# Optimization experiments

Hardware: AMD Instinct MI355X
Metric: run time of the kernel (lower is better)

Reference implementation:

```python
import jax, jax.numpy as jnp
import numpy as np

VOCAB, D_MODEL, N_HEADS, D_FF = 32000, 2048, 16, 8192
B, S = 2, 2048
HEAD_DIM = D_MODEL // N_HEADS
EPS = 1e-6


def setup_inputs() -> dict:
    key = jax.random.key(0)
    ks = jax.random.split(key, 12)
    sc = 0.02
    return {
        "tokens": jax.random.randint(ks[0], (B, S), 0, VOCAB),
        "tok_emb": jax.random.normal(ks[1], (VOCAB, D_MODEL), jnp.float32) * sc,
        "wq": jax.random.normal(ks[2], (D_MODEL, D_MODEL), jnp.float32) * sc,
        "wk": jax.random.normal(ks[3], (D_MODEL, D_MODEL), jnp.float32) * sc,
        "wv": jax.random.normal(ks[4], (D_MODEL, D_MODEL), jnp.float32) * sc,
        "wo": jax.random.normal(ks[5], (D_MODEL, D_MODEL), jnp.float32) * sc,
        "attn_norm_w": jnp.ones((D_MODEL,), jnp.float32),
        "ffn_norm_w": jnp.ones((D_MODEL,), jnp.float32),
        "final_norm_w": jnp.ones((D_MODEL,), jnp.float32),
        "w1": jax.random.normal(ks[6], (D_FF, D_MODEL), jnp.float32) * sc,
        "w2": jax.random.normal(ks[7], (D_MODEL, D_FF), jnp.float32) * sc,
        "out_proj": jax.random.normal(ks[8], (VOCAB, D_MODEL), jnp.float32) * sc,
    }


def rms_norm(x, w):
    return w * x * jax.lax.rsqrt(jnp.mean(x * x, axis=-1, keepdims=True) + EPS)


def reference(tokens, tok_emb, wq, wk, wv, wo, attn_norm_w, ffn_norm_w,
              final_norm_w, w1, w2, out_proj):
    x = tok_emb[tokens]  # [B, S, D]
    b, s, _ = x.shape

    # --- attention (explicit causal QK^T + softmax, as in source) ---
    xn = rms_norm(x, attn_norm_w)
    q = (xn @ wq.T).reshape(b, s, N_HEADS, HEAD_DIM)
    k = (xn @ wk.T).reshape(b, s, N_HEADS, HEAD_DIM)
    v = (xn @ wv.T).reshape(b, s, N_HEADS, HEAD_DIM)
    scores = jnp.einsum("bqhd,bkhd->bhqk", q, k) * (HEAD_DIM ** -0.5)
    causal = jnp.triu(jnp.ones((s, s), dtype=bool), k=1)  # True above diag
    scores = jnp.where(causal, -jnp.inf, scores)
    attn = jax.nn.softmax(scores, axis=-1)
    out = jnp.einsum("bhqk,bkhd->bqhd", attn, v).reshape(b, s, -1)
    x = x + out @ wo.T

    # --- FFN (world_size=1: all_gather/reduce_scatter are identities) ---
    hn = rms_norm(x, ffn_norm_w)
    h = jax.nn.silu(hn @ w1.T) @ w2.T
    x = x + h

    logits = rms_norm(x, final_norm_w) @ out_proj.T  # [B, S, VOCAB]
    return logits
```

## Files before the change

### kernel.cpp

```cpp
#include <hip/hip_runtime.h>
#include <stdint.h>

#define DM     2048
#define NHE    16
#define DFF    8192
#define NBATCH 2
#define SEQ    2048
#define NTOK   4096
#define HD     128
#define NVOCAB 32000

typedef __attribute__((ext_vector_type(8))) short short8;
typedef __attribute__((ext_vector_type(4))) float f32x4;
typedef __attribute__((ext_vector_type(4))) unsigned short u16x4;

static __device__ __forceinline__ unsigned short f2b(float f) {
  union { float f; uint32_t u; } v; v.f = f;
  return (unsigned short)((v.u + 0x7FFFu + ((v.u >> 16) & 1u)) >> 16);
}

static __device__ __forceinline__ void gload16(const void* g, void* l) {
  __builtin_amdgcn_global_load_lds(
      (const __attribute__((address_space(1))) unsigned int*)g,
      (__attribute__((address_space(3))) unsigned int*)l, 16, 0, 0);
}

__global__ void k_f32_to_bf16(const float* __restrict__ in,
                              unsigned short* __restrict__ out, int nq) {
  int i = blockIdx.x * blockDim.x + threadIdx.x;
  int stride = gridDim.x * blockDim.x;
  for (; i < nq; i += stride) {
    float4 v = ((const float4*)in)[i];
    u16x4 o;
    o.x = f2b(v.x); o.y = f2b(v.y); o.z = f2b(v.z); o.w = f2b(v.w);
    ((u16x4*)out)[i] = o;
  }
}

__global__ void k_embed(const int* __restrict__ tok,
                        const float* __restrict__ emb, float* __restrict__ x) {
  int n = blockIdx.x;
  int t = tok[n];
  const float4* src = (const float4*)(emb + (size_t)t * DM);
  float4* dst = (float4*)(x + (size_t)n * DM);
  for (int i = threadIdx.x; i < DM / 4; i += blockDim.x) dst[i] = src[i];
}

__global__ void k_rmsnorm(const float* __restrict__ x, const float* __restrict__ wt,
                          unsigned short* __restrict__ out) {
  int n = blockIdx.x;
  const float* row = x + (size_t)n * DM;
  float ss = 0.f;
  #pragma unroll
  for (int it = 0; it < 2; ++it) {
    int i = threadIdx.x * 4 + it * 1024;
    float4 v = *(const float4*)(row + i);
    ss += v.x * v.x + v.y * v.y + v.z * v.z + v.w * v.w;
  }
  #pragma unroll
  for (int m = 1; m < 64; m <<= 1) ss += __shfl_xor(ss, m);
  __shared__ float p[4];
  if ((threadIdx.x & 63) == 0) p[threadIdx.x >> 6] = ss;
  __syncthreads();
  float inv = rsqrtf((p[0] + p[1] + p[2] + p[3]) * (1.f / DM) + 1e-6f);
  #pragma unroll
  for (int it = 0; it < 2; ++it) {
    int i = threadIdx.x * 4 + it * 1024;
    float4 v = *(const float4*)(row + i);
    float4 w4 = *(const float4*)(wt + i);
    u16x4 o;
    o.x = f2b(v.x * w4.x * inv); o.y = f2b(v.y * w4.y * inv);
    o.z = f2b(v.z * w4.z * inv); o.w = f2b(v.w * w4.w * inv);
    *(u16x4*)(out + (size_t)n * DM + i) = o;
  }
}

#define EPI_BF16  0
#define EPI_RESID 1
#define EPI_SILU  2
#define EPI_F32   3

template <int EPI>
__launch_bounds__(512, 2)
__global__ void k_gemm_nt(const unsigned short* __restrict__ A,
                          const unsigned short* __restrict__ Bm,
                          int M, int N, int K,
                          float* __restrict__ Cf, unsigned short* __restrict__ Cb,
                          const float* __restrict__ R) {
  __shared__ unsigned short lds[2][32768];
  int nbn = N >> 8;
  int nwg = gridDim.x;
  int bid = blockIdx.x;
  int cpx = nwg >> 3;
  bid = (bid & 7) * cpx + (bid >> 3);
  int bm = bid / nbn, bn = bid % nbn;
  int t = threadIdx.x, w = t >> 6, lane = t & 63;
  int wr = w >> 2, wc = w & 3;
  int g = lane >> 4, l15 = lane & 15;

  f32x4 acc[8][4] = {};

  size_t abase = (size_t)(bm * 256) * K;
  size_t bbase = (size_t)(bn * 256) * K;
  int nkt = K >> 6;

  auto stage = [&](int buf, int kt) {
    unsigned short* dst = lds[buf];
    int k0 = kt << 6;
    #pragma unroll
    for (int i = 0; i < 4; ++i) {
      int pos = (i * 512 + t) << 4;
      int row = pos >> 7, colb = pos & 127;
      int csrc = colb ^ ((row & 7) << 4);
      gload16(A + abase + (size_t)row * K + k0 + (csrc >> 1), (char*)dst + pos);
    }
    #pragma unroll
    for (int i = 0; i < 4; ++i) {
      int pos = (i * 512 + t) << 4;
      int row = pos >> 7, colb = pos & 127;
      int csrc = colb ^ ((row & 7) << 4);
      gload16(Bm + bbase + (size_t)row * K + k0 + (csrc >> 1),
              (char*)(dst + 16384) + pos);
    }
  };

  stage(0, 0);
  for (int kt = 0; kt < nkt; ++kt) {
    int cur = kt & 1;
    if (kt + 1 < nkt) {
      stage(1 - cur, kt + 1);
      asm volatile("s_waitcnt vmcnt(8)" ::: "memory");
    } else {
      asm volatile("s_waitcnt vmcnt(0)" ::: "memory");
    }
    __builtin_amdgcn_s_barrier();
    __builtin_amdgcn_sched_barrier(0);

    const unsigned short* abuf = lds[cur];
    const unsigned short* bbuf = abuf + 16384;
    __builtin_amdgcn_s_setprio(1);
    #pragma unroll
    for (int kk = 0; kk < 2; ++kk) {
      short8 af[8], bfr[4];
      #pragma unroll
      for (int mm = 0; mm < 8; ++mm) {
        int row = wr * 128 + mm * 16 + l15;
        int col = kk * 64 + g * 16;
        af[mm] = *(const short8*)((const char*)abuf + row * 128 + (col ^ ((row & 7) << 4)));
      }
      #pragma unroll
      for (int nn = 0; nn < 4; ++nn) {
        int row = wc * 64 + nn * 16 + l15;
        int col = kk * 64 + g * 16;
        bfr[nn] = *(const short8*)((const char*)bbuf + row * 128 + (col ^ ((row & 7) << 4)));
      }
      #pragma unroll
      for (int mm = 0; mm < 8; ++mm)
        #pragma unroll
        for (int nn = 0; nn < 4; ++nn)
          acc[mm][nn] = __builtin_amdgcn_mfma_f32_16x16x32_bf16(af[mm], bfr[nn], acc[mm][nn], 0, 0, 0);
    }
    __builtin_amdgcn_s_setprio(0);
    __builtin_amdgcn_sched_barrier(0);
    __builtin_amdgcn_s_barrier();
  }

  #pragma unroll
  for (int mm = 0; mm < 8; ++mm) {
    #pragma unroll
    for (int nn = 0; nn < 4; ++nn) {
      #pragma unroll
      for (int r = 0; r < 4; ++r) {
        int grow = bm * 256 + wr * 128 + mm * 16 + g * 4 + r;
        int gcol = bn * 256 + wc * 64 + nn * 16 + l15;
        size_t off = (size_t)grow * N + gcol;
        float v = acc[mm][nn][r];
        if (EPI == EPI_BF16) {
          Cb[off] = f2b(v);
        } else if (EPI == EPI_RESID) {
          Cf[off] = R[off] + v;
        } else if (EPI == EPI_SILU) {
          float s = 1.f / (1.f + __expf(-v));
          Cb[off] = f2b(v * s);
        } else {
          Cf[off] = v;
        }
      }
    }
  }
}

__global__ void k_transpose_v(const unsigned short* __restrict__ v, int vstride,
                              unsigned short* __restrict__ vt) {
  __shared__ unsigned short tile[64][136];
  int pr = blockIdx.x >> 5;
  int st = blockIdx.x & 31;
  int bb = pr >> 4, h = pr & 15;
  int row = threadIdx.x >> 2;
  int cq = threadIdx.x & 3;
  const unsigned short* src =
      v + (size_t)(bb * SEQ + st * 64 + row) * vstride + h * HD + cq * 32;
  #pragma unroll
  for (int j = 0; j < 4; ++j)
    *(short8*)&tile[row][cq * 32 + j * 8] = *(const short8*)(src + j * 8);
  __syncthreads();
  int d = threadIdx.x >> 1;
  int sh = threadIdx.x & 1;
  unsigned short tmp[32];
  #pragma unroll
  for (int j = 0; j < 32; ++j) tmp[j] = tile[sh * 32 + j][d];
  unsigned short* dst = vt + ((size_t)pr * HD + d) * SEQ + st * 64 + sh * 32;
  #pragma unroll
  for (int j = 0; j < 4; ++j)
    *(short8*)(dst + j * 8) = *(const short8*)&tmp[j * 8];
}

__launch_bounds__(256)
__global__ void k_attn(const unsigned short* __restrict__ q,
                       const unsigned short* __restrict__ k,
                       const unsigned short* __restrict__ vt,
                       unsigned short* __restrict__ ao, int qk_stride) {
  __shared__ unsigned short k_lds[64 * 128];
  __shared__ unsigned short vt_lds[128 * 64];
  __shared__ unsigned short p_lds[4][32 * 64];

  int bid = blockIdx.x;
  int pr = bid >> 4;
  int qt = 15 - (bid & 15);
  int bb = pr >> 4, h = pr & 15;
  int t = threadIdx.x, w = t >> 6, lane = t & 63;
  int g = lane >> 4, l15 = lane & 15;
  const float SCL = 0.08838834764831845f * 1.4426950408889634f;

  int qrow_base = qt * 128 + w * 32;
  short8 aq[2][4];
  #pragma unroll
  for (int mm = 0; mm < 2; ++mm) {
    size_t n = (size_t)(bb * SEQ + qrow_base + mm * 16 + l15);
    #pragma unroll
    for (int kk = 0; kk < 4; ++kk)
      aq[mm][kk] = *(const short8*)(q + n * qk_stride + h * HD + kk * 32 + g * 8);
  }

  f32x4 o[2][8] = {};
  float m2[2][4], ls[2][4];
  #pragma unroll
  for (int mm = 0; mm < 2; ++mm)
    #pragma unroll
    for (int r = 0; r < 4; ++r) { m2[mm][r] = -1e30f; ls[mm][r] = 0.f; }

  int nkv = 2 * qt + 2;
  for (int kvt = 0; kvt < nkv; ++kvt) {
    #pragma unroll
    for (int i = 0; i < 4; ++i) {
      int pos = ((i * 4 + w) << 10) + lane * 16;
      {
        int row = pos >> 8, csw = pos & 255;
        int csrc = csw ^ ((row & 7) << 4);
        gload16(k + (size_t)(bb * SEQ + kvt * 64 + row) * qk_stride + h * HD + (csrc >> 1),
                (char*)k_lds + ((i * 4 + w) << 10));
      }
      {
        int row = pos >> 7, csw = pos & 127;
        int csrc = csw ^ ((row & 7) << 4);
        gload16(vt + ((size_t)pr * HD + row) * SEQ + kvt * 64 + (csrc >> 1),
                (char*)vt_lds + ((i * 4 + w) << 10));
      }
    }
    __syncthreads();

    f32x4 s[2][4] = {};
    #pragma unroll
    for (int kk = 0; kk < 4; ++kk) {
      short8 bk[4];
      #pragma unroll
      for (int nn = 0; nn < 4; ++nn) {
        int row = nn * 16 + l15;
        int col = kk * 64 + g * 16;
        bk[nn] = *(const short8*)((const char*)k_lds + row * 256 + (col ^ ((row & 7) << 4)));
      }
      #pragma unroll
      for (int mm = 0; mm < 2; ++mm)
        #pragma unroll
        for (int nn = 0; nn < 4; ++nn)
          s[mm][nn] = __builtin_amdgcn_mfma_f32_16x16x32_bf16(aq[mm][kk], bk[nn], s[mm][nn], 0, 0, 0);
    }

    bool diag = (kvt >= 2 * qt);
    #pragma unroll
    for (int mm = 0; mm < 2; ++mm) {
      float mx[4] = {-1e30f, -1e30f, -1e30f, -1e30f};
      #pragma unroll
      for (int nn = 0; nn < 4; ++nn)
        #pragma unroll
        for (int r = 0; r < 4; ++r) {
          float sv = s[mm][nn][r] * SCL;
          if (diag) {
            int kvg = kvt * 64 + nn * 16 + l15;
            int qg = qrow_base + mm * 16 + g * 4 + r;
            if (kvg > qg) sv = -1e30f;
          }
          s[mm][nn][r] = sv;
          mx[r] = fmaxf(mx[r], sv);
        }
      #pragma unroll
      for (int r = 0; r < 4; ++r) {
        mx[r] = fmaxf(mx[r], __shfl_xor(mx[r], 1));
        mx[r] = fmaxf(mx[r], __shfl_xor(mx[r], 2));
        mx[r] = fmaxf(mx[r], __shfl_xor(mx[r], 4));
        mx[r] = fmaxf(mx[r], __shfl_xor(mx[r], 8));
        float mn = fmaxf(m2[mm][r], mx[r]);
        float al = exp2f(m2[mm][r] - mn);
        m2[mm][r] = mn;
        ls[mm][r] *= al;
        #pragma unroll
        for (int dd = 0; dd < 8; ++dd) o[mm][dd][r] *= al;
      }
      #pragma unroll
      for (int nn = 0; nn < 4; ++nn)
        #pragma unroll
        for (int r = 0; r < 4; ++r) {
          float pv = exp2f(s[mm][nn][r] - m2[mm][r]);
          ls[mm][r] += pv;
          int row = mm * 16 + g * 4 + r;
          int colb = (nn * 16 + l15) * 2;
          *(unsigned short*)((char*)p_lds[w] + row * 128 + (colb ^ (((row >> 1) & 7) << 4))) = f2b(pv);
        }
    }

    #pragma unroll
    for (int kk = 0; kk < 2; ++kk) {
      short8 pf[2], vf[8];
      #pragma unroll
      for (int mm = 0; mm < 2; ++mm) {
        int row = mm * 16 + l15;
        int col = kk * 64 + g * 16;
        pf[mm] = *(const short8*)((const char*)p_lds[w] + row * 128 + (col ^ (((row >> 1) & 7) << 4)));
      }
      #pragma unroll
      for (int dd = 0; dd < 8; ++dd) {
        int row = dd * 16 + l15;
        int col = kk * 64 + g * 16;
        vf[dd] = *(const short8*)((const char*)vt_lds + row * 128 + (col ^ ((row & 7) << 4)));
      }
      #pragma unroll
      for (int mm = 0; mm < 2; ++mm)
        #pragma unroll
        for (int dd = 0; dd < 8; ++dd)
          o[mm][dd] = __builtin_amdgcn_mfma_f32_16x16x32_bf16(pf[mm], vf[dd], o[mm][dd], 0, 0, 0);
    }
    __syncthreads();
  }

  #pragma unroll
  for (int mm = 0; mm < 2; ++mm) {
    float inv[4];
    #pragma unroll
    for (int r = 0; r < 4; ++r) {
      float tt = ls[mm][r];
      tt += __shfl_xor(tt, 1);
      tt += __shfl_xor(tt, 2);
      tt += __shfl_xor(tt, 4);
      tt += __shfl_xor(tt, 8);
      inv[r] = 1.f / tt;
    }
    #pragma unroll
    for (int dd = 0; dd < 8; ++dd)
      #pragma unroll
      for (int r = 0; r < 4; ++r) {
        size_t n = (size_t)(bb * SEQ + qrow_base + mm * 16 + g * 4 + r);
        int col = h * HD + dd * 16 + l15;
        ao[n * DM + col] = f2b(o[mm][dd][r] * inv[r]);
      }
  }
}

extern "C" void kernel_launch(void* const* d_in, const int* in_sizes, int n_in,
                              void* d_out, int out_size, void* d_ws, size_t ws_size,
                              hipStream_t stream) {
  const int* tokens = (const int*)d_in[0];
  const float* tok_emb = (const float*)d_in[1];
  const float* wq = (const float*)d_in[2];
  const float* wk = (const float*)d_in[3];
  const float* wv = (const float*)d_in[4];
  const float* wo = (const float*)d_in[5];
  const float* attn_nw = (const float*)d_in[6];
  const float* ffn_nw = (const float*)d_in[7];
  const float* final_nw = (const float*)d_in[8];
  const float* w1 = (const float*)d_in[9];
  const float* w2 = (const float*)d_in[10];
  const float* out_proj = (const float*)d_in[11];
  float* out = (float*)d_out;

  char* ws = (char*)d_ws;
  size_t off = 0;
  auto alloc = [&](size_t bytes) -> char* {
    char* p = ws + off;
    off += (bytes + 255) & ~(size_t)255;
    return p;
  };
  unsigned short* wqkv_b = (unsigned short*)alloc((size_t)3 * DM * DM * 2);
  unsigned short* wo_b = (unsigned short*)alloc((size_t)DM * DM * 2);
  unsigned short* w1_b = (unsigned short*)alloc((size_t)DFF * DM * 2);
  unsigned short* w2_b = (unsigned short*)alloc((size_t)DM * DFF * 2);
  unsigned short* wop_b = (unsigned short*)alloc((size_t)NVOCAB * DM * 2);
  float* x = (float*)alloc((size_t)NTOK * DM * 4);
  unsigned short* xn = (unsigned short*)alloc((size_t)NTOK * DM * 2);
  unsigned short* qkv_b = (unsigned short*)alloc((size_t)NTOK * 3 * DM * 2);
  unsigned short* vt_b = (unsigned short*)alloc((size_t)NTOK * DM * 2);
  unsigned short* ao_b = (unsigned short*)alloc((size_t)NTOK * DM * 2);
  unsigned short* h1_b = qkv_b;

  auto conv = [&](const float* src, unsigned short* dst, size_t n) {
    int nq = (int)(n / 4);
    int grid = (nq + 255) / 256;
    if (grid > 4096) grid = 4096;
    k_f32_to_bf16<<<grid, 256, 0, stream>>>(src, dst, nq);
  };
  conv(wq, wqkv_b, (size_t)DM * DM);
  conv(wk, wqkv_b + (size_t)DM * DM, (size_t)DM * DM);
  conv(wv, wqkv_b + (size_t)2 * DM * DM, (size_t)DM * DM);
  conv(wo, wo_b, (size_t)DM * DM);
  conv(w1, w1_b, (size_t)DFF * DM);
  conv(w2, w2_b, (size_t)DM * DFF);
  conv(out_proj, wop_b, (size_t)NVOCAB * DM);

  k_embed<<<NTOK, 256, 0, stream>>>(tokens, tok_emb, x);
  k_rmsnorm<<<NTOK, 256, 0, stream>>>(x, attn_nw, xn);

  k_gemm_nt<EPI_BF16><<<(NTOK / 256) * (3 * DM / 256), 512, 0, stream>>>(
      xn, wqkv_b, NTOK, 3 * DM, DM, nullptr, qkv_b, nullptr);

  k_transpose_v<<<32 * 32, 256, 0, stream>>>(qkv_b + 2 * DM, 3 * DM, vt_b);
  k_attn<<<32 * 16, 256, 0, stream>>>(qkv_b, qkv_b + DM, vt_b, ao_b, 3 * DM);

  k_gemm_nt<EPI_RESID><<<(NTOK / 256) * (DM / 256), 512, 0, stream>>>(
      ao_b, wo_b, NTOK, DM, DM, x, nullptr, x);

  k_rmsnorm<<<NTOK, 256, 0, stream>>>(x, ffn_nw, xn);
  k_gemm_nt<EPI_SILU><<<(NTOK / 256) * (DFF / 256), 512, 0, stream>>>(
      xn, w1_b, NTOK, DFF, DM, nullptr, h1_b, nullptr);
  k_gemm_nt<EPI_RESID><<<(NTOK / 256) * (DM / 256), 512, 0, stream>>>(
      h1_b, w2_b, NTOK, DM, DFF, x, nullptr, x);

  k_rmsnorm<<<NTOK, 256, 0, stream>>>(x, final_nw, xn);
  k_gemm_nt<EPI_F32><<<(NTOK / 256) * (NVOCAB / 256), 512, 0, stream>>>(
      xn, wop_b, NTOK, NVOCAB, DM, out, nullptr, nullptr);
}
```

Before: 1.458 ms.

## Add phased-prefetch GEMM with grouped tiles and a 128-row GEMM for N=2048 projections

Replaces the GEMM with a variant that splits each K-tile into four phases, interleaving next-tile global loads into LDS with MFMA compute. It also remaps block ids into column groups (GN) for better L2 reuse. A separate 128x256-tile kernel serves the N=2048 output projections to raise block count, and logits are written with nontemporal stores. Extra barriers per phase and weaker overlap are the added risks.

```diff
diff --git a/kernel.cpp b/kernel.cpp
--- a/kernel.cpp
+++ b/kernel.cpp
@@ -80,88 +80,125 @@
 #define EPI_SILU  2
 #define EPI_F32   3
 
+#define PHASE(Q, VM)                                                          \
+  {                                                                           \
+    short8 af[2][2];                                                          \
+    _Pragma("unroll")                                                         \
+    for (int mi = 0; mi < 2; ++mi)                                            \
+      _Pragma("unroll")                                                       \
+      for (int kk = 0; kk < 2; ++kk) {                                        \
+        int row = wr * 128 + (2 * (Q) + mi) * 16 + l15;                       \
+        int col = kk * 64 + g * 16;                                           \
+        af[mi][kk] = *(const short8*)((const char*)abuf + row * 128 +         \
+                                      (col ^ ((row & 7) << 4)));              \
+      }                                                                       \
+    if ((Q) == 0) {                                                           \
+      _Pragma("unroll")                                                       \
+      for (int nn = 0; nn < 4; ++nn)                                          \
+        _Pragma("unroll")                                                     \
+        for (int kk = 0; kk < 2; ++kk) {                                      \
+          int row = wc * 64 + nn * 16 + l15;                                  \
+          int col = kk * 64 + g * 16;                                         \
+          bfr[nn][kk] = *(const short8*)((const char*)bbuf + row * 128 +      \
+                                         (col ^ ((row & 7) << 4)));           \
+        }                                                                     \
+    }                                                                         \
+    if (kt + 1 < nkt) {                                                       \
+      if ((Q) == 0) {                                                         \
+        _Pragma("unroll")                                                     \
+        for (int i = 0; i < 4; ++i) {                                         \
+          int pos = (i * 512 + t) << 4;                                       \
+          int row = pos >> 7, colb = pos & 127;                               \
+          int csrc = colb ^ ((row & 7) << 4);                                 \
+          gload16(Bm + bbase + (size_t)row * K + k0n + (csrc >> 1),           \
+                  (char*)(nbuf + 16384) + pos);                               \
+        }                                                                     \
+      }                                                                       \
+      {                                                                       \
+        int pos = (t < 256) ? ((Q) * 4096 + t * 16)                           \
+                            : (16384 + (Q) * 4096 + (t - 256) * 16);          \
+        int row = pos >> 7, colb = pos & 127;                                 \
+        int csrc = colb ^ ((row & 7) << 4);                                   \
+        gload16(A + abase + (size_t)row * K + k0n + (csrc >> 1),              \
+                (char*)nbuf + pos);                                           \
+      }                                                                       \
+      asm volatile("s_waitcnt vmcnt(" VM ")" ::: "memory");                   \
+    } else {                                                                  \
+      if ((Q) == 0) asm volatile("s_waitcnt vmcnt(0)" ::: "memory");          \
+    }                                                                         \
+    __builtin_amdgcn_s_barrier();                                             \
+    asm volatile("s_waitcnt lgkmcnt(0)" ::: "memory");                        \
+    __builtin_amdgcn_sched_barrier(0);                                        \
+    __builtin_amdgcn_s_setprio(1);                                            \
+    _Pragma("unroll")                                                         \
+    for (int mi = 0; mi < 2; ++mi)                                            \
+      _Pragma("unroll")                                                       \
+      for (int nn = 0; nn < 4; ++nn)                                          \
+        _Pragma("unroll")                                                     \
+        for (int kk = 0; kk < 2; ++kk)                                        \
+          acc[2 * (Q) + mi][nn] = __builtin_amdgcn_mfma_f32_16x16x32_bf16(    \
+              af[mi][kk], bfr[nn][kk], acc[2 * (Q) + mi][nn], 0, 0, 0);       \
+    __builtin_amdgcn_s_setprio(0);                                            \
+    __builtin_amdgcn_sched_barrier(0);                                        \
+  }
+
 template <int EPI>
 __launch_bounds__(512, 2)
-__global__ void k_gemm_nt(const unsigned short* __restrict__ A,
-                          const unsigned short* __restrict__ Bm,
-                          int M, int N, int K,
-                          float* __restrict__ Cf, unsigned short* __restrict__ Cb,
-                          const float* __restrict__ R) {
+__global__ void k_gemm8p(const unsigned short* __restrict__ A,
+                         const unsigned short* __restrict__ Bm,
+                         int M, int N, int K, int GN,
+                         float* __restrict__ Cf, unsigned short* __restrict__ Cb,
+                         const float* __restrict__ R) {
   __shared__ unsigned short lds[2][32768];
-  int nbn = N >> 8;
+  int nbm = M >> 8;
   int nwg = gridDim.x;
   int bid = blockIdx.x;
   int cpx = nwg >> 3;
   bid = (bid & 7) * cpx + (bid >> 3);
-  int bm = bid / nbn, bn = bid % nbn;
+  int grpsz = nbm * GN;
+  int gg = bid / grpsz, rr = bid % grpsz;
+  int bm = rr / GN;
+  int bn = gg * GN + rr % GN;
   int t = threadIdx.x, w = t >> 6, lane = t & 63;
   int wr = w >> 2, wc = w & 3;
   int g = lane >> 4, l15 = lane & 15;
 
   f32x4 acc[8][4] = {};
-
   size_t abase = (size_t)(bm * 256) * K;
   size_t bbase = (size_t)(bn * 256) * K;
   int nkt = K >> 6;
 
-  auto stage = [&](int buf, int kt) {
-    unsigned short* dst = lds[buf];
-    int k0 = kt << 6;
+  {
+    unsigned short* nbuf = lds[0];
     #pragma unroll
     for (int i = 0; i < 4; ++i) {
       int pos = (i * 512 + t) << 4;
       int row = pos >> 7, colb = pos & 127;
       int csrc = colb ^ ((row & 7) << 4);
-      gload16(A + abase + (size_t)row * K + k0 + (csrc >> 1), (char*)dst + pos);
+      gload16(Bm + bbase + (size_t)row * K + (csrc >> 1), (char*)(nbuf + 16384) + pos);
     }
     #pragma unroll
     for (int i = 0; i < 4; ++i) {
       int pos = (i * 512 + t) << 4;
       int row = pos >> 7, colb = pos & 127;
       int csrc = colb ^ ((row & 7) << 4);
-      gload16(Bm + bbase + (size_t)row * K + k0 + (csrc >> 1),
-              (char*)(dst + 16384) + pos);
-    }
-  };
-
-  stage(0, 0);
+      gload16(A + abase + (size_t)row * K + (csrc >> 1), (char*)nbuf + pos);
+    }
+    asm volatile("s_waitcnt vmcnt(0)" ::: "memory");
+    __builtin_amdgcn_s_barrier();
+  }
+
   for (int kt = 0; kt < nkt; ++kt) {
     int cur = kt & 1;
-    if (kt + 1 < nkt) {
-      stage(1 - cur, kt + 1);
-      asm volatile("s_waitcnt vmcnt(8)" ::: "memory");
-    } else {
-      asm volatile("s_waitcnt vmcnt(0)" ::: "memory");
-    }
-    __builtin_amdgcn_s_barrier();
-    __builtin_amdgcn_sched_barrier(0);
-
     const unsigned short* abuf = lds[cur];
     const unsigned short* bbuf = abuf + 16384;
-    __builtin_amdgcn_s_setprio(1);
-    #pragma unroll
-    for (int kk = 0; kk < 2; ++kk) {
-      short8 af[8], bfr[4];
-      #pragma unroll
-      for (int mm = 0; mm < 8; ++mm) {
-        int row = wr * 128 + mm * 16 + l15;
-        int col = kk * 64 + g * 16;
-        af[mm] = *(const short8*)((const char*)abuf + row * 128 + (col ^ ((row & 7) << 4)));
-      }
-      #pragma unroll
-      for (int nn = 0; nn < 4; ++nn) {
-        int row = wc * 64 + nn * 16 + l15;
-        int col = kk * 64 + g * 16;
-        bfr[nn] = *(const short8*)((const char*)bbuf + row * 128 + (col ^ ((row & 7) << 4)));
-      }
-      #pragma unroll
-      for (int mm = 0; mm < 8; ++mm)
-        #pragma unroll
-        for (int nn = 0; nn < 4; ++nn)
-          acc[mm][nn] = __builtin_amdgcn_mfma_f32_16x16x32_bf16(af[mm], bfr[nn], acc[mm][nn], 0, 0, 0);
-    }
-    __builtin_amdgcn_s_setprio(0);
-    __builtin_amdgcn_sched_barrier(0);
+    unsigned short* nbuf = lds[1 - cur];
+    int k0n = (kt + 1) << 6;
+    short8 bfr[4][2];
+    PHASE(0, "7")
+    PHASE(1, "7")
+    PHASE(2, "7")
+    PHASE(3, "3")
     __builtin_amdgcn_s_barrier();
   }
 
@@ -183,7 +220,116 @@
           float s = 1.f / (1.f + __expf(-v));
           Cb[off] = f2b(v * s);
         } else {
-          Cf[off] = v;
+          __builtin_nontemporal_store(v, &Cf[off]);
+        }
+      }
+    }
+  }
+}
+
+template <int EPI>
+__launch_bounds__(512, 2)
+__global__ void k_gemm_sm(const unsigned short* __restrict__ A,
+                          const unsigned short* __restrict__ Bm,
+                          int M, int N, int K,
+                          float* __restrict__ Cf, unsigned short* __restrict__ Cb,
+                          const float* __restrict__ R) {
+  __shared__ unsigned short lds[2][24576];
+  int nbn = N >> 8;
+  int nwg = gridDim.x;
+  int bid = blockIdx.x;
+  int cpx = nwg >> 3;
+  bid = (bid & 7) * cpx + (bid >> 3);
+  int bm = bid / nbn, bn = bid % nbn;
+  int t = threadIdx.x, w = t >> 6, lane = t & 63;
+  int wr = w >> 2, wc = w & 3;
+  int g = lane >> 4, l15 = lane & 15;
+
+  f32x4 acc[4][4] = {};
+  size_t abase = (size_t)(bm * 128) * K;
+  size_t bbase = (size_t)(bn * 256) * K;
+  int nkt = K >> 6;
+
+  auto stage = [&](int buf, int kt) {
+    unsigned short* dst = lds[buf];
+    int k0 = kt << 6;
+    #pragma unroll
+    for (int i = 0; i < 2; ++i) {
+      int pos = (i * 512 + t) << 4;
+      int row = pos >> 7, colb = pos & 127;
+      int csrc = colb ^ ((row & 7) << 4);
+      gload16(A + abase + (size_t)row * K + k0 + (csrc >> 1), (char*)dst + pos);
+    }
+    #pragma unroll
+    for (int i = 0; i < 4; ++i) {
+      int pos = (i * 512 + t) << 4;
+      int row = pos >> 7, colb = pos & 127;
+      int csrc = colb ^ ((row & 7) << 4);
+      gload16(Bm + bbase + (size_t)row * K + k0 + (csrc >> 1),
+              (char*)(dst + 8192) + pos);
+    }
+  };
+
+  stage(0, 0);
+  for (int kt = 0; kt < nkt; ++kt) {
+    int cur = kt & 1;
+    if (kt + 1 < nkt) {
+      stage(1 - cur, kt + 1);
+      asm volatile("s_waitcnt vmcnt(6)" ::: "memory");
+    } else {
+      asm volatile("s_waitcnt vmcnt(0)" ::: "memory");
+    }
+    __builtin_amdgcn_s_barrier();
+    __builtin_amdgcn_sched_barrier(0);
+
+    const unsigned short* abuf = lds[cur];
+    const unsigned short* bbuf = abuf + 8192;
+    __builtin_amdgcn_s_setprio(1);
+    #pragma unroll
+    for (int kk = 0; kk < 2; ++kk) {
+      short8 af[4], bfr[4];
+      #pragma unroll
+      for (int mm = 0; mm < 4; ++mm) {
+        int row = wr * 64 + mm * 16 + l15;
+        int col = kk * 64 + g * 16;
+        af[mm] = *(const short8*)((const char*)abuf + row * 128 + (col ^ ((row & 7) << 4)));
+      }
+      #pragma unroll
+      for (int nn = 0; nn < 4; ++nn) {
+        int row = wc * 64 + nn * 16 + l15;
+        int col = kk * 64 + g * 16;
+        bfr[nn] = *(const short8*)((const char*)bbuf + row * 128 + (col ^ ((row & 7) << 4)));
+      }
+      #pragma unroll
+      for (int mm = 0; mm < 4; ++mm)
+        #pragma unroll
+        for (int nn = 0; nn < 4; ++nn)
+          acc[mm][nn] = __builtin_amdgcn_mfma_f32_16x16x32_bf16(af[mm], bfr[nn], acc[mm][nn], 0, 0, 0);
+    }
+    __builtin_amdgcn_s_setprio(0);
+    __builtin_amdgcn_sched_barrier(0);
+    __builtin_amdgcn_s_barrier();
+  }
+
+  #pragma unroll
+  for (int mm = 0; mm < 4; ++mm) {
+    #pragma unroll
+    for (int nn = 0; nn < 4; ++nn) {
+      #pragma unroll
+      for (int r = 0; r < 4; ++r) {
+        int grow = bm * 128 + wr * 64 + mm * 16 + g * 4 + r;
+        int gcol = bn * 256 + wc * 64 + nn * 16 + l15;
+        size_t off = (size_t)grow * N + gcol;
+        float v = acc[mm][nn][r];
+        if (EPI == EPI_BF16) {
+          Cb[off] = f2b(v);
+        } else if (EPI == EPI_RESID) {
+          Cf[off] = R[off] + v;
+        } else if (EPI == EPI_SILU) {
+          float s = 1.f / (1.f + __expf(-v));
+          Cb[off] = f2b(v * s);
+        } else {
+          __builtin_nontemporal_store(v, &Cf[off]);
         }
       }
     }
@@ -428,22 +574,22 @@
   k_embed<<<NTOK, 256, 0, stream>>>(tokens, tok_emb, x);
   k_rmsnorm<<<NTOK, 256, 0, stream>>>(x, attn_nw, xn);
 
-  k_gemm_nt<EPI_BF16><<<(NTOK / 256) * (3 * DM / 256), 512, 0, stream>>>(
-      xn, wqkv_b, NTOK, 3 * DM, DM, nullptr, qkv_b, nullptr);
+  k_gemm8p<EPI_BF16><<<(NTOK / 256) * (3 * DM / 256), 512, 0, stream>>>(
+      xn, wqkv_b, NTOK, 3 * DM, DM, 3 * DM / 256, nullptr, qkv_b, nullptr);
 
   k_transpose_v<<<32 * 32, 256, 0, stream>>>(qkv_b + 2 * DM, 3 * DM, vt_b);
   k_attn<<<32 * 16, 256, 0, stream>>>(qkv_b, qkv_b + DM, vt_b, ao_b, 3 * DM);
 
-  k_gemm_nt<EPI_RESID><<<(NTOK / 256) * (DM / 256), 512, 0, stream>>>(
+  k_gemm_sm<EPI_RESID><<<(NTOK / 128) * (DM / 256), 512, 0, stream>>>(
       ao_b, wo_b, NTOK, DM, DM, x, nullptr, x);
 
   k_rmsnorm<<<NTOK, 256, 0, stream>>>(x, ffn_nw, xn);
-  k_gemm_nt<EPI_SILU><<<(NTOK / 256) * (DFF / 256), 512, 0, stream>>>(
-      xn, w1_b, NTOK, DFF, DM, nullptr, h1_b, nullptr);
-  k_gemm_nt<EPI_RESID><<<(NTOK / 256) * (DM / 256), 512, 0, stream>>>(
+  k_gemm8p<EPI_SILU><<<(NTOK / 256) * (DFF / 256), 512, 0, stream>>>(
+      xn, w1_b, NTOK, DFF, DM, DFF / 256, nullptr, h1_b, nullptr);
+  k_gemm_sm<EPI_RESID><<<(NTOK / 128) * (DM / 256), 512, 0, stream>>>(
       h1_b, w2_b, NTOK, DM, DFF, x, nullptr, x);
 
   k_rmsnorm<<<NTOK, 256, 0, stream>>>(x, final_nw, xn);
-  k_gemm_nt<EPI_F32><<<(NTOK / 256) * (NVOCAB / 256), 512, 0, stream>>>(
-      xn, wop_b, NTOK, NVOCAB, DM, out, nullptr, nullptr);
-}
+  k_gemm8p<EPI_F32><<<(NTOK / 256) * (NVOCAB / 256), 512, 0, stream>>>(
+      xn, wop_b, NTOK, NVOCAB, DM, 25, out, nullptr, nullptr);
+}
```

After: 1.316 ms. -9.8%, faster.
